# Performance work log

Hardware: AMD Instinct MI355X
Metric: run time of the kernel (lower is better)

The kernel has to match this reference:

```python
import jax, jax.numpy as jnp
import numpy as np

NUM_HEADS = 8

def setup_inputs() -> dict:
    key = jax.random.key(0)
    k1, k2, k3, k4 = jax.random.split(key, 4)
    B, C, H, W = 8, 512, 32, 32
    x = jax.random.normal(k1, (B, C, H, W), dtype=jnp.float32)
    # Conv2d 1x1 weights flattened to [out, in]
    w_qkv = jax.random.normal(k2, (3 * C, C), dtype=jnp.float32) * (C ** -0.5)
    w_proj = jax.random.normal(k3, (C, C), dtype=jnp.float32) * (C ** -0.5)
    b_proj = jax.random.normal(k4, (C,), dtype=jnp.float32) * 0.02
    return {"x": x, "w_qkv": w_qkv, "w_proj": w_proj, "b_proj": b_proj}

def reference(x, w_qkv, w_proj, b_proj):
    B, C, H, W = x.shape
    nh = NUM_HEADS
    hd = C // nh
    N = H * W
    scale = hd ** -0.5
    xf = x.reshape(B, C, N)
    # 1x1 conv == per-pixel GEMM; reshape 3C channels as (nh, 3*hd) per torch reshape
    qkv = jnp.einsum('oc,bcn->bon', w_qkv, xf).reshape(B, nh, 3 * hd, N)
    q, k, v = jnp.split(qkv, 3, axis=2)  # each [B, nh, hd, N]
    # attn[b,h,nk,nq] = sum_d k[b,h,d,nk] * q[b,h,d,nq]
    attn = jnp.einsum('bhdn,bhdm->bhnm', k, q) * scale
    attn = jax.nn.softmax(attn, axis=-2)  # softmax over key axis (dim=-2), as in source
    out = jnp.einsum('bhdn,bhnm->bhdm', v, attn).reshape(B, C, H, W)
    out = jnp.einsum('oc,bchw->bohw', w_proj, out) + b_proj[None, :, None, None]
    return out
```

## Files before the change

kernel.cpp:

```cpp
#include <hip/hip_runtime.h>
#include <math.h>


typedef unsigned int u32;
typedef float  f32x4 __attribute__((ext_vector_type(4)));
typedef short  s16x8 __attribute__((ext_vector_type(8)));
typedef unsigned short u16x4 __attribute__((ext_vector_type(4)));
typedef unsigned int   u32x2 __attribute__((ext_vector_type(2)));
typedef unsigned int   u32x4 __attribute__((ext_vector_type(4)));

#define MFMA16(a, b, c) __builtin_amdgcn_mfma_f32_16x16x32_bf16(a, b, c, 0, 0, 0)

__device__ __forceinline__ ushort f2bf(float f) {
    u32 b = __float_as_uint(f);
    return (ushort)((b + 0x7FFFu + ((b >> 16) & 1u)) >> 16);
}
__device__ __forceinline__ float bf2f(ushort v) {
    return __uint_as_float(((u32)v) << 16);
}
__device__ __forceinline__ u32 cvtpk(float a, float b) {
    u32 r;
    asm("v_cvt_pk_bf16_f32 %0, %1, %2" : "=v"(r) : "v"(a), "v"(b));
    return r;
}

__global__ __launch_bounds__(256) void prep(
    const float* __restrict__ x, const float* __restrict__ wq,
    const float* __restrict__ wp, ushort* __restrict__ xh,
    ushort* __restrict__ wq_s, ushort* __restrict__ wp_s) {
    __shared__ __align__(16) ushort Th[64 * 72];
    const int t = threadIdx.x;

    {
        const int id = (blockIdx.z * 8 + blockIdx.y) * 16 + blockIdx.x;
        size_t base = ((size_t)id * 256 + t) * 4;
        const float* src; ushort* dst; size_t off;
        if (base < 786432) { src = wq; dst = wq_s; off = base; }
        else               { src = wp; dst = wp_s; off = base - 786432; }
        f32x4 v = *(const f32x4*)(src + off);
        u16x4 s;
#pragma unroll
        for (int e = 0; e < 4; e++) s[e] = f2bf(v[e]);
        *(u16x4*)(dst + off) = s;
    }

    const int n0 = blockIdx.x * 64, c0 = blockIdx.y * 64, b = blockIdx.z;
    const int c = t >> 2, nseg = (t & 3) * 4;
    const float* src = x + ((size_t)b * 512 + c0 + c) * 1024 + n0;
#pragma unroll
    for (int i = 0; i < 4; i++) {
        f32x4 v = *(const f32x4*)(src + nseg + i * 16);
#pragma unroll
        for (int e = 0; e < 4; e++) {
            int nl = nseg + i * 16 + e;
            Th[nl * 72 + c] = f2bf(v[e]);
        }
    }
    __syncthreads();
#pragma unroll
    for (int i = 0; i < 2; i++) {
        int nl = i * 32 + (t >> 3);
        int u = t & 7;
        s16x8 vh = *(const s16x8*)(Th + nl * 72 + u * 8);
        size_t go = ((size_t)b * 1024 + n0 + nl) * 512 + c0 + u * 8;
        *(s16x8*)(xh + go) = vh;
    }
}

__device__ __forceinline__ void gemm_core64(
    const ushort* __restrict__ A_g, int arow0,
    const ushort* __restrict__ B_g, size_t brow0,
    ushort* smem, f32x4 (&acc)[4][4]) {
    const int t = threadIdx.x;
    ushort* As = smem;
    ushort* Bs = smem + 9216;
    const int ro = t >> 1, cs = (t & 1) << 5;
    const size_t ga = (size_t)(arow0 + ro) * 512 + cs;
    const size_t gb = (brow0 + ro) * 512 + cs;
    const int l15 = t & 15, quad = (t >> 4) & 3, wv = t >> 6;
    const int lra = (((wv >> 1) * 64) + l15) * 72 + quad * 8;
    const int lrb = (((wv & 1) * 64) + l15) * 72 + quad * 8;
    const int lw = ro * 72 + cs;

    s16x8 va[4], vb[4];
#pragma unroll
    for (int e = 0; e < 4; e++) {
        va[e] = *(const s16x8*)(A_g + ga + e * 8);
        vb[e] = *(const s16x8*)(B_g + gb + e * 8);
    }

    for (int k0 = 0; k0 < 512; k0 += 64) {
        __syncthreads();
#pragma unroll
        for (int e = 0; e < 4; e++) {
            *(s16x8*)(As + lw + e * 8) = va[e];
            *(s16x8*)(Bs + lw + e * 8) = vb[e];
        }
        const int kn = (k0 + 64) & 511;
#pragma unroll
        for (int e = 0; e < 4; e++) {
            va[e] = *(const s16x8*)(A_g + ga + kn + e * 8);
            vb[e] = *(const s16x8*)(B_g + gb + kn + e * 8);
        }
        __syncthreads();
#pragma unroll
        for (int kk = 0; kk < 2; kk++) {
            s16x8 a[4], bb[4];
#pragma unroll
            for (int Mt = 0; Mt < 4; Mt++)
                a[Mt] = *(const s16x8*)(As + lra + kk * 32 + Mt * 1152);
#pragma unroll
            for (int Nt = 0; Nt < 4; Nt++)
                bb[Nt] = *(const s16x8*)(Bs + lrb + kk * 32 + Nt * 1152);
#pragma unroll
            for (int Mt = 0; Mt < 4; Mt++)
#pragma unroll
                for (int Nt = 0; Nt < 4; Nt++)
                    acc[Mt][Nt] = MFMA16(a[Mt], bb[Nt], acc[Mt][Nt]);
        }
    }
    __syncthreads();
}

__global__ __launch_bounds__(256) void gemm_qkv(
    const ushort* __restrict__ wq_s, const ushort* __restrict__ xt_h,
    ushort* __restrict__ qT, ushort* __restrict__ kT, ushort* __restrict__ vT) {
    __shared__ __align__(16) ushort smem[18432];
    f32x4 acc[4][4];
#pragma unroll
    for (int i = 0; i < 4; i++)
#pragma unroll
        for (int j = 0; j < 4; j++) acc[i][j] = (f32x4)0.0f;

    const int n0 = blockIdx.x * 128, o0 = blockIdx.y * 128, bz = blockIdx.z;
    gemm_core64(wq_s, o0, xt_h, (size_t)bz * 1024 + n0, smem, acc);

    const int t = threadIdx.x;
    const int l15 = t & 15, quad = (t >> 4) & 3, wv = t >> 6, lane = t & 63;
    const int g = blockIdx.y * 2 + (wv >> 1);
    const int role = g % 3, head = g / 3;
    const int nh = (wv & 1) * 64;
    const size_t hb = (size_t)bz * 8 + head;
    const float scale = (role == 0) ? 0.18033688011112042f : 1.0f;

    if (role < 2) {
        ushort* dst = (role == 0) ? qT : kT;
        ushort* T = smem + wv * 2304;
        const size_t rowbase = hb * 1024 + n0 + nh;
#pragma unroll
        for (int sp = 0; sp < 2; sp++) {
#pragma unroll
            for (int Mti = 0; Mti < 2; Mti++)
#pragma unroll
                for (int Nt = 0; Nt < 4; Nt++) {
                    f32x4 v = acc[sp * 2 + Mti][Nt];
                    u32x2 pk;
                    pk.x = cvtpk(v[0] * scale, v[1] * scale);
                    pk.y = cvtpk(v[2] * scale, v[3] * scale);
                    *(u32x2*)(T + (Nt * 16 + l15) * 36 + Mti * 16 + quad * 4) = pk;
                }
            asm volatile("s_waitcnt lgkmcnt(0)" ::: "memory");
#pragma unroll
            for (int i = 0; i < 8; i++) {
                int nl = i * 8 + (lane >> 3);
                u16x4 vv = *(const u16x4*)(T + nl * 36 + (lane & 7) * 4);
                *(u16x4*)(dst + (rowbase + nl) * 64 + sp * 32 + (lane & 7) * 4) = vv;
            }
            asm volatile("s_waitcnt lgkmcnt(0)" ::: "memory");
        }
    } else {
        const size_t vb2 = hb * 64 * 1024 + (size_t)(n0 + nh);
#pragma unroll
        for (int Mt = 0; Mt < 4; Mt++)
#pragma unroll
            for (int Nt = 0; Nt < 4; Nt++)
#pragma unroll
                for (int r = 0; r < 4; r++)
                    vT[vb2 + (size_t)(Mt * 16 + quad * 4 + r) * 1024 + Nt * 16 + l15] =
                        f2bf(acc[Mt][Nt][r]);
    }
}

__global__ __launch_bounds__(256) void gemm_proj(
    const ushort* __restrict__ wp_s, const ushort* __restrict__ ht,
    const float* __restrict__ bias, float* __restrict__ out) {
    __shared__ __align__(16) ushort smem[18432];
    f32x4 acc[4][4];
#pragma unroll
    for (int i = 0; i < 4; i++)
#pragma unroll
        for (int j = 0; j < 4; j++) acc[i][j] = (f32x4)0.0f;

    const int n0 = blockIdx.x * 128, o0 = blockIdx.y * 128, bz = blockIdx.z;
    gemm_core64(wp_s, o0, ht, (size_t)bz * 1024 + n0, smem, acc);

    const int t = threadIdx.x;
    const int l15 = t & 15, quad = (t >> 4) & 3, wv = t >> 6;
#pragma unroll
    for (int Mt = 0; Mt < 4; Mt++)
#pragma unroll
        for (int Nt = 0; Nt < 4; Nt++) {
            int ob = o0 + (wv >> 1) * 64 + Mt * 16 + quad * 4;
            int nn = n0 + (wv & 1) * 64 + Nt * 16 + l15;
#pragma unroll
            for (int r = 0; r < 4; r++)
                out[((size_t)bz * 512 + ob + r) * 1024 + nn] = acc[Mt][Nt][r] + bias[ob + r];
        }
}

__global__ __launch_bounds__(256, 2) void attn_mfma(
    const ushort* __restrict__ qT, const ushort* __restrict__ kT,
    const ushort* __restrict__ vT, ushort* __restrict__ ht) {
    __shared__ __align__(16) ushort Ps[4 * 4352];
    __shared__ float Ls[4][64];
    const int t = threadIdx.x;
    const int id = blockIdx.x + (blockIdx.y << 4);
    const int swz = (id & 7) * 128 + (id >> 3);
    const int qt = swz & 15, bh = swz >> 4;
    const int b = bh >> 3, h = bh & 7;
    const int m0 = qt * 64;
    const int l15 = t & 15, quad = (t >> 4) & 3, wv = t >> 6;

    s16x8 qf[4][2];
#pragma unroll
    for (int Nt = 0; Nt < 4; Nt++) {
        const size_t qb = ((size_t)bh * 1024 + m0 + Nt * 16 + l15) * 64 + quad * 8;
        qf[Nt][0] = *(const s16x8*)(qT + qb);
        qf[Nt][1] = *(const s16x8*)(qT + qb + 32);
    }

    f32x4 O[4][4];
#pragma unroll
    for (int i = 0; i < 4; i++)
#pragma unroll
        for (int j = 0; j < 4; j++) O[i][j] = (f32x4)0.0f;
    float lrun[4] = {0.f, 0.f, 0.f, 0.f};

    const ushort* kb = kT + (size_t)bh * 65536;
    const ushort* vb = vT + (size_t)bh * 65536;
    ushort* Pw = Ps + wv * 4352;

    s16x8 kf[2][4], vf[2][4];
    {
        const int kt = wv * 4;
        const size_t kbase = (size_t)kt * 4096 + l15 * 64 + quad * 8;
        const size_t vbase = (size_t)l15 * 1024 + kt * 64 + quad * 8;
#pragma unroll
        for (int ks = 0; ks < 2; ks++)
#pragma unroll
            for (int Mt = 0; Mt < 4; Mt++) {
                kf[ks][Mt] = *(const s16x8*)(kb + kbase + Mt * 1024 + ks * 32);
                vf[ks][Mt] = *(const s16x8*)(vb + vbase + Mt * 16384 + ks * 32);
            }
    }

#pragma unroll 1
    for (int i = 0; i < 4; i++) {
        const int ktn = wv * 4 + i + 1;

#pragma unroll
        for (int g2 = 0; g2 < 2; g2++) {
            f32x4 S[4][2];
#pragma unroll
            for (int a = 0; a < 4; a++) { S[a][0] = (f32x4)0.0f; S[a][1] = (f32x4)0.0f; }
            __builtin_amdgcn_s_setprio(1);
#pragma unroll
            for (int ks = 0; ks < 2; ks++)
#pragma unroll
                for (int Mt = 0; Mt < 4; Mt++)
#pragma unroll
                    for (int n2 = 0; n2 < 2; n2++)
                        S[Mt][n2] = MFMA16(kf[ks][Mt], qf[g2 * 2 + n2][ks], S[Mt][n2]);
            __builtin_amdgcn_s_setprio(0);

            if (g2 == 1 && i < 3) {
                const size_t kbase = (size_t)ktn * 4096 + l15 * 64 + quad * 8;
#pragma unroll
                for (int ks = 0; ks < 2; ks++)
#pragma unroll
                    for (int Mt = 0; Mt < 4; Mt++)
                        kf[ks][Mt] = *(const s16x8*)(kb + kbase + Mt * 1024 + ks * 32);
            }

#pragma unroll
            for (int n2 = 0; n2 < 2; n2++) {
#pragma unroll
                for (int Mt = 0; Mt < 4; Mt++)
#pragma unroll
                    for (int r = 0; r < 4; r++)
                        S[Mt][n2][r] = __builtin_amdgcn_exp2f(S[Mt][n2][r]);
                float s0 = (S[0][n2][0] + S[0][n2][1]) + (S[0][n2][2] + S[0][n2][3]);
                float s1 = (S[1][n2][0] + S[1][n2][1]) + (S[1][n2][2] + S[1][n2][3]);
                float s2 = (S[2][n2][0] + S[2][n2][1]) + (S[2][n2][2] + S[2][n2][3]);
                float s3 = (S[3][n2][0] + S[3][n2][1]) + (S[3][n2][2] + S[3][n2][3]);
                lrun[g2 * 2 + n2] += (s0 + s1) + (s2 + s3);
            }
#pragma unroll
            for (int Mt = 0; Mt < 4; Mt++)
#pragma unroll
                for (int n2 = 0; n2 < 2; n2++) {
                    u32x2 pb;
                    pb.x = cvtpk(S[Mt][n2][0], S[Mt][n2][1]);
                    pb.y = cvtpk(S[Mt][n2][2], S[Mt][n2][3]);
                    *(u32x2*)(Pw + ((g2 * 2 + n2) * 16 + l15) * 68 + Mt * 16 + quad * 4) = pb;
                }
        }

#pragma unroll
        for (int ks = 0; ks < 2; ks++) {
            s16x8 pf[4];
#pragma unroll
            for (int Nt = 0; Nt < 4; Nt++)
                pf[Nt] = *(const s16x8*)(Pw + (Nt * 16 + l15) * 68 + ks * 32 + quad * 8);
            __builtin_amdgcn_s_setprio(1);
#pragma unroll
            for (int Mt = 0; Mt < 4; Mt++)
#pragma unroll
                for (int Nt = 0; Nt < 4; Nt++)
                    O[Mt][Nt] = MFMA16(vf[ks][Mt], pf[Nt], O[Mt][Nt]);
            __builtin_amdgcn_s_setprio(0);
        }

        if (i < 3) {
            const size_t vbase = (size_t)l15 * 1024 + ktn * 64 + quad * 8;
#pragma unroll
            for (int ks = 0; ks < 2; ks++)
#pragma unroll
                for (int Mt = 0; Mt < 4; Mt++)
                    vf[ks][Mt] = *(const s16x8*)(vb + vbase + Mt * 16384 + ks * 32);
        }
    }

#pragma unroll
    for (int Mt = 0; Mt < 4; Mt++)
#pragma unroll
        for (int Nt = 0; Nt < 4; Nt++) {
            u32x2 pk;
            pk.x = cvtpk(O[Mt][Nt][0], O[Mt][Nt][1]);
            pk.y = cvtpk(O[Mt][Nt][2], O[Mt][Nt][3]);
            *(u32x2*)(Pw + (Nt * 16 + l15) * 68 + Mt * 16 + quad * 4) = pk;
        }
#pragma unroll
    for (int Nt = 0; Nt < 4; Nt++) {
        float ts = lrun[Nt];
        ts += __shfl_xor(ts, 16);
        ts += __shfl_xor(ts, 32);
        if (quad == 0) Ls[wv][Nt * 16 + l15] = ts;
    }
    __syncthreads();

    const int q = t >> 2, ds = (t & 3) * 16;
    const float l = Ls[0][q] + Ls[1][q] + Ls[2][q] + Ls[3][q];
    const float linv = 1.f / l;
    float acc[16];
#pragma unroll
    for (int e = 0; e < 16; e++) acc[e] = 0.f;
#pragma unroll
    for (int w = 0; w < 4; w++) {
        s16x8 a0 = *(const s16x8*)(Ps + w * 4352 + q * 68 + ds);
        s16x8 a1 = *(const s16x8*)(Ps + w * 4352 + q * 68 + ds + 8);
#pragma unroll
        for (int e = 0; e < 8; e++) {
            acc[e] += bf2f((ushort)a0[e]);
            acc[8 + e] += bf2f((ushort)a1[e]);
        }
    }
    u32x4 r0, r1;
#pragma unroll
    for (int e = 0; e < 4; e++) {
        r0[e] = cvtpk(acc[2 * e] * linv, acc[2 * e + 1] * linv);
        r1[e] = cvtpk(acc[8 + 2 * e] * linv, acc[9 + 2 * e] * linv);
    }
    const size_t go = ((size_t)b * 1024 + m0 + q) * 512 + h * 64 + ds;
    *(u32x4*)(ht + go) = r0;
    *(u32x4*)(ht + go + 8) = r1;
}

extern "C" void kernel_launch(void* const* d_in, const int* in_sizes, int n_in,
                              void* d_out, int out_size, void* d_ws, size_t ws_size,
                              hipStream_t stream) {
    (void)in_sizes; (void)n_in; (void)out_size; (void)ws_size;
    const float* x      = (const float*)d_in[0];
    const float* w_qkv  = (const float*)d_in[1];
    const float* w_proj = (const float*)d_in[2];
    const float* b_proj = (const float*)d_in[3];
    float* out = (float*)d_out;

    char* ws = (char*)d_ws;
    ushort* xt_h = (ushort*)(ws);
    ushort* wq_s = (ushort*)(ws + 8388608);
    ushort* wp_s = (ushort*)(ws + 9961472);
    ushort* qT   = (ushort*)(ws + 10485760);
    ushort* kT   = (ushort*)(ws + 18874368);
    ushort* vT   = (ushort*)(ws + 27262976);
    ushort* ht   = xt_h;

    prep<<<dim3(16, 8, 8), 256, 0, stream>>>(x, w_qkv, w_proj, xt_h,
                                             wq_s, wp_s);
    gemm_qkv<<<dim3(8, 12, 8), 256, 0, stream>>>(wq_s, xt_h, qT, kT, vT);
    attn_mfma<<<dim3(16, 64), 256, 0, stream>>>(qT, kT, vT, ht);
    gemm_proj<<<dim3(8, 4, 8), 256, 0, stream>>>(wp_s, xt_h, b_proj, out);
}
```

Baseline: 148.4 us.

## Use async global-to-LDS loads with double-buffered swizzled tiles in GEMM core

Replaces the register-staged GEMM mainloop with direct global_load_lds transfers into two LDS buffers of K=32 each, alternating between them so the next tile's load runs during the current tile's MFMAs. The LDS layout drops the padded 72-stride rows for an unpadded 32-stride layout with an XOR swizzle to avoid bank conflicts. This removes the VGPR staging and the LDS store instructions, at the cost of twice as many barriers and a full vmcnt(0) wait per half-iteration, which may expose load latency.

```diff
diff --git a/kernel.cpp b/kernel.cpp
--- a/kernel.cpp
+++ b/kernel.cpp
@@ -22,6 +22,11 @@
     u32 r;
     asm("v_cvt_pk_bf16_f32 %0, %1, %2" : "=v"(r) : "v"(a), "v"(b));
     return r;
+}
+__device__ __forceinline__ void gload_lds16(const ushort* g, ushort* l) {
+    __builtin_amdgcn_global_load_lds(
+        (const __attribute__((address_space(1))) unsigned int*)g,
+        (__attribute__((address_space(3))) unsigned int*)l, 16, 0, 0);
 }
 
 __global__ __launch_bounds__(256) void prep(
@@ -67,65 +72,91 @@
     }
 }
 
-__device__ __forceinline__ void gemm_core64(
+__device__ __forceinline__ void gemm_core_async(
     const ushort* __restrict__ A_g, int arow0,
     const ushort* __restrict__ B_g, size_t brow0,
     ushort* smem, f32x4 (&acc)[4][4]) {
     const int t = threadIdx.x;
-    ushort* As = smem;
-    ushort* Bs = smem + 9216;
-    const int ro = t >> 1, cs = (t & 1) << 5;
-    const size_t ga = (size_t)(arow0 + ro) * 512 + cs;
-    const size_t gb = (brow0 + ro) * 512 + cs;
     const int l15 = t & 15, quad = (t >> 4) & 3, wv = t >> 6;
-    const int lra = (((wv >> 1) * 64) + l15) * 72 + quad * 8;
-    const int lrb = (((wv & 1) * 64) + l15) * 72 + quad * 8;
-    const int lw = ro * 72 + cs;
-
-    s16x8 va[4], vb[4];
-#pragma unroll
-    for (int e = 0; e < 4; e++) {
-        va[e] = *(const s16x8*)(A_g + ga + e * 8);
-        vb[e] = *(const s16x8*)(B_g + gb + e * 8);
-    }
-
-    for (int k0 = 0; k0 < 512; k0 += 64) {
-        __syncthreads();
-#pragma unroll
-        for (int e = 0; e < 4; e++) {
-            *(s16x8*)(As + lw + e * 8) = va[e];
-            *(s16x8*)(Bs + lw + e * 8) = vb[e];
-        }
-        const int kn = (k0 + 64) & 511;
-#pragma unroll
-        for (int e = 0; e < 4; e++) {
-            va[e] = *(const s16x8*)(A_g + ga + kn + e * 8);
-            vb[e] = *(const s16x8*)(B_g + gb + kn + e * 8);
-        }
-        __syncthreads();
-#pragma unroll
-        for (int kk = 0; kk < 2; kk++) {
+    const int lane = t & 63;
+
+    const int srow = wv * 32 + (lane >> 2);
+    const int sk = ((lane & 3) ^ ((lane >> 3) & 3)) * 8;
+    const size_t gA0 = (size_t)(arow0 + srow) * 512 + sk;
+    const size_t gA1 = (size_t)(arow0 + srow + 16) * 512 + sk;
+    const size_t gB0 = (brow0 + srow) * 512 + sk;
+    const size_t gB1 = (brow0 + srow + 16) * 512 + sk;
+    const int lb = wv * 1024;
+
+    const int sq = quad ^ ((l15 >> 1) & 3);
+    const int lra = (((wv >> 1) * 64) + l15) * 32 + sq * 8;
+    const int lrb = (((wv & 1) * 64) + l15) * 32 + sq * 8;
+
+    ushort* A0 = smem;
+    ushort* B0 = smem + 4096;
+    ushort* A1 = smem + 8192;
+    ushort* B1 = smem + 12288;
+
+    gload_lds16(A_g + gA0, A0 + lb);
+    gload_lds16(A_g + gA1, A0 + lb + 512);
+    gload_lds16(B_g + gB0, B0 + lb);
+    gload_lds16(B_g + gB1, B0 + lb + 512);
+    asm volatile("s_waitcnt vmcnt(0)" ::: "memory");
+    __syncthreads();
+
+#pragma unroll 1
+    for (int j = 0; j < 16; j += 2) {
+        {
+            const int kn = (j + 1) * 32;
+            gload_lds16(A_g + gA0 + kn, A1 + lb);
+            gload_lds16(A_g + gA1 + kn, A1 + lb + 512);
+            gload_lds16(B_g + gB0 + kn, B1 + lb);
+            gload_lds16(B_g + gB1 + kn, B1 + lb + 512);
             s16x8 a[4], bb[4];
 #pragma unroll
             for (int Mt = 0; Mt < 4; Mt++)
-                a[Mt] = *(const s16x8*)(As + lra + kk * 32 + Mt * 1152);
+                a[Mt] = *(const s16x8*)(A0 + lra + Mt * 512);
 #pragma unroll
             for (int Nt = 0; Nt < 4; Nt++)
-                bb[Nt] = *(const s16x8*)(Bs + lrb + kk * 32 + Nt * 1152);
+                bb[Nt] = *(const s16x8*)(B0 + lrb + Nt * 512);
 #pragma unroll
             for (int Mt = 0; Mt < 4; Mt++)
 #pragma unroll
                 for (int Nt = 0; Nt < 4; Nt++)
                     acc[Mt][Nt] = MFMA16(a[Mt], bb[Nt], acc[Mt][Nt]);
-        }
-    }
-    __syncthreads();
+            asm volatile("s_waitcnt vmcnt(0)" ::: "memory");
+            __syncthreads();
+        }
+        {
+            if (j + 2 < 16) {
+                const int kn = (j + 2) * 32;
+                gload_lds16(A_g + gA0 + kn, A0 + lb);
+                gload_lds16(A_g + gA1 + kn, A0 + lb + 512);
+                gload_lds16(B_g + gB0 + kn, B0 + lb);
+                gload_lds16(B_g + gB1 + kn, B0 + lb + 512);
+            }
+            s16x8 a[4], bb[4];
+#pragma unroll
+            for (int Mt = 0; Mt < 4; Mt++)
+                a[Mt] = *(const s16x8*)(A1 + lra + Mt * 512);
+#pragma unroll
+            for (int Nt = 0; Nt < 4; Nt++)
+                bb[Nt] = *(const s16x8*)(B1 + lrb + Nt * 512);
+#pragma unroll
+            for (int Mt = 0; Mt < 4; Mt++)
+#pragma unroll
+                for (int Nt = 0; Nt < 4; Nt++)
+                    acc[Mt][Nt] = MFMA16(a[Mt], bb[Nt], acc[Mt][Nt]);
+            asm volatile("s_waitcnt vmcnt(0)" ::: "memory");
+            __syncthreads();
+        }
+    }
 }
 
 __global__ __launch_bounds__(256) void gemm_qkv(
     const ushort* __restrict__ wq_s, const ushort* __restrict__ xt_h,
     ushort* __restrict__ qT, ushort* __restrict__ kT, ushort* __restrict__ vT) {
-    __shared__ __align__(16) ushort smem[18432];
+    __shared__ __align__(16) ushort smem[16384];
     f32x4 acc[4][4];
 #pragma unroll
     for (int i = 0; i < 4; i++)
@@ -133,7 +164,7 @@
         for (int j = 0; j < 4; j++) acc[i][j] = (f32x4)0.0f;
 
     const int n0 = blockIdx.x * 128, o0 = blockIdx.y * 128, bz = blockIdx.z;
-    gemm_core64(wq_s, o0, xt_h, (size_t)bz * 1024 + n0, smem, acc);
+    gemm_core_async(wq_s, o0, xt_h, (size_t)bz * 1024 + n0, smem, acc);
 
     const int t = threadIdx.x;
     const int l15 = t & 15, quad = (t >> 4) & 3, wv = t >> 6, lane = t & 63;
@@ -184,7 +215,7 @@
 __global__ __launch_bounds__(256) void gemm_proj(
     const ushort* __restrict__ wp_s, const ushort* __restrict__ ht,
     const float* __restrict__ bias, float* __restrict__ out) {
-    __shared__ __align__(16) ushort smem[18432];
+    __shared__ __align__(16) ushort smem[16384];
     f32x4 acc[4][4];
 #pragma unroll
     for (int i = 0; i < 4; i++)
@@ -192,7 +223,7 @@
         for (int j = 0; j < 4; j++) acc[i][j] = (f32x4)0.0f;
 
     const int n0 = blockIdx.x * 128, o0 = blockIdx.y * 128, bz = blockIdx.z;
-    gemm_core64(wp_s, o0, ht, (size_t)bz * 1024 + n0, smem, acc);
+    gemm_core_async(wp_s, o0, ht, (size_t)bz * 1024 + n0, smem, acc);
 
     const int t = threadIdx.x;
     const int l15 = t & 15, quad = (t >> 4) & 3, wv = t >> 6;
```

After: 150.4 us. About the same (+1.4%).
